# Kernel tuning notes

Measured on AMD Instinct MI355X. Metric: run time of the kernel, lower is better.

Reference implementation:

```python
import jax, jax.numpy as jnp
import numpy as np

H = 32        # num query heads
KVH = 8       # num kv heads
D = 128       # head_dim
ROPE_BASE = 10000.0
NEG_INF = jnp.finfo(jnp.float32).min


def rope_interleaved(x):
    """Interleaved (GPT-NeoX-style pairs (x0,x1),(x2,x3),...) RoPE. x: [b,s,h,d]."""
    d = x.shape[-1]
    inv_freq = 1.0 / (ROPE_BASE ** (jnp.arange(0, d, 2, dtype=jnp.float32) / d))  # [d/2]
    pos = jnp.arange(x.shape[1], dtype=jnp.float32)
    ang = pos[:, None] * inv_freq[None, :]                    # [s, d/2]
    cos = jnp.cos(ang)[None, :, None, :]
    sin = jnp.sin(ang)[None, :, None, :]
    xp = x.reshape(*x.shape[:-1], d // 2, 2)
    x1, x2 = xp[..., 0], xp[..., 1]
    r1 = x1 * cos - x2 * sin
    r2 = x1 * sin + x2 * cos
    return jnp.stack([r1, r2], axis=-1).reshape(x.shape)


def setup_inputs() -> dict:
    key = jax.random.key(0)
    k1, k2, k3 = jax.random.split(key, 3)
    B, S, E = 2, 2048, 4096
    x = jax.random.normal(k1, (B, S, E), dtype=jnp.float32)
    wqkv = jax.random.normal(k2, (E + 2 * KVH * D, E), dtype=jnp.float32) * 0.02
    wo = jax.random.normal(k3, (E, E), dtype=jnp.float32) * 0.02
    return {"x": x, "wqkv": wqkv, "wo": wo}


def reference(x, wqkv, wo):
    b, s, e = x.shape
    q_per_kv = H // KVH
    # fused QKV projection (torch Linear layout: y = x @ W.T)
    qkv = jnp.einsum('bse,fe->bsf', x, wqkv)
    # rearrange 'b s (h gs d) -> b s h gs d', gs = q_per_kv + 2
    qkv = qkv.reshape(b, s, KVH, q_per_kv + 2, D)
    q = qkv[..., :q_per_kv, :].reshape(b, s, H, D)   # (h gs) -> H query heads
    k = qkv[..., -2, :]                              # [b,s,KVH,D]
    v = qkv[..., -1, :]
    # RoPE (rotary_emb_dim == head_dim, interleaved)
    q = rope_interleaved(q)
    k = rope_interleaved(k)
    # GQA: expand kv heads to match query heads
    k = jnp.repeat(k, q_per_kv, axis=2)              # [b,s,H,D]
    v = jnp.repeat(v, q_per_kv, axis=2)
    scale = D ** -0.5
    scores = jnp.einsum('bqhd,bkhd->bhqk', q, k) * scale
    causal = jnp.tril(jnp.ones((s, s), dtype=bool))
    scores = jnp.where(causal[None, None], scores, NEG_INF)
    attn = jax.nn.softmax(scores, axis=-1)
    ctx = jnp.einsum('bhqk,bkhd->bqhd', attn, v).reshape(b, s, H * D)
    return jnp.einsum('bsf,ef->bse', ctx, wo)
```

## Files before the change

### kernel.cpp

```cpp
#include <hip/hip_runtime.h>
#include <cstdint>

typedef __bf16 bf16;
typedef __bf16 bf16x8 __attribute__((ext_vector_type(8)));
typedef float  f32x4  __attribute__((ext_vector_type(4)));

#define AS1(p) ((__attribute__((address_space(1))) void*)(p))
#define AS3(p) ((__attribute__((address_space(3))) void*)(p))

__device__ __forceinline__ void gload16(const void* g, void* l) {
  __builtin_amdgcn_global_load_lds(AS1(g), AS3(l), 16, 0, 0);
}

constexpr int B_ = 2, S_ = 2048, E_ = 4096, H_ = 32, KVH_ = 8, D_ = 128;
constexpr int QPK_ = H_ / KVH_;
constexpr int F_ = E_ + 2 * KVH_ * D_;
constexpr int M_ = B_ * S_;

__global__ void f2bf_k(const float* __restrict__ in, bf16* __restrict__ out, int n8) {
  int i = blockIdx.x * 256 + threadIdx.x;
  if (i >= n8) return;
  const float4* p = (const float4*)(in + (size_t)i * 8);
  float4 a = p[0], b = p[1];
  bf16x8 o;
  o[0] = (bf16)a.x; o[1] = (bf16)a.y; o[2] = (bf16)a.z; o[3] = (bf16)a.w;
  o[4] = (bf16)b.x; o[5] = (bf16)b.y; o[6] = (bf16)b.z; o[7] = (bf16)b.w;
  *(bf16x8*)(out + (size_t)i * 8) = o;
}

__global__ void rope_table_k(float2* __restrict__ tab) {
  int i = blockIdx.x * 256 + threadIdx.x;
  int s = i >> 6, f = i & 63;
  float inv = powf(10000.0f, -2.0f * (float)f / 128.0f);
  float ang = (float)s * inv;
  tab[i] = make_float2(cosf(ang), sinf(ang));
}

template <typename OutT>
__global__ __launch_bounds__(512, 2)
void gemm256(const bf16* __restrict__ A, const bf16* __restrict__ B,
             OutT* __restrict__ C, int M, int N, int K) {
  __shared__ bf16 As[2][16384];
  __shared__ bf16 Bs[2][16384];
  const int tid = threadIdx.x;
  const int wid = tid >> 6, lane = tid & 63;
  const int l15 = lane & 15, g = lane >> 4;
  const int wr = wid >> 2, wc = wid & 3;
  const int bm = blockIdx.x, bn = blockIdx.y;
  const bf16* Ab = A + (size_t)bm * 256 * K;
  const bf16* Bb = B + (size_t)bn * 256 * K;
  const int nT = K >> 6;
  const int swzr = (l15 & 7) << 4;

  f32x4 acc[8][4];
#pragma unroll
  for (int m = 0; m < 8; ++m)
#pragma unroll
    for (int n = 0; n < 4; ++n) acc[m][n] = (f32x4){0.f, 0.f, 0.f, 0.f};

  auto stg = [&](const bf16* src, bf16* dst, int t, int h) {
#pragma unroll
    for (int i = 0; i < 2; ++i) {
      int lb = h * 16384 + i * 8192 + wid * 1024 + lane * 16;
      int row = lb >> 7;
      int colb = (lb & 127) ^ ((row & 7) << 4);
      gload16(src + (size_t)row * K + t * 64 + (colb >> 1),
              dst + ((h * 16384 + i * 8192 + wid * 1024) >> 1));
    }
  };

  bf16x8 af[4][2];
  bf16x8 bfr[2][2][2];

  stg(Bb, Bs[0], 0, 0); stg(Bb, Bs[0], 0, 1);
  stg(Ab, As[0], 0, 0); stg(Ab, As[0], 0, 1);
  if (nT > 1) {
    stg(Bb, Bs[1], 1, 0); stg(Bb, Bs[1], 1, 1);
    asm volatile("s_waitcnt vmcnt(4)");
  } else {
    asm volatile("s_waitcnt vmcnt(0)");
  }
  __builtin_amdgcn_sched_barrier(0);
  __builtin_amdgcn_s_barrier();

  auto tileK = [&](int t, const int cur) {
#pragma unroll
    for (int m = 0; m < 4; ++m) {
      int arow = wr * 128 + m * 16 + l15;
#pragma unroll
      for (int ks = 0; ks < 2; ++ks)
        af[m][ks] = *(const bf16x8*)&As[cur][(arow << 6) + (((ks * 64 + g * 16) ^ swzr) >> 1)];
    }
#pragma unroll
    for (int n = 0; n < 2; ++n) {
      int brow = wc * 64 + n * 16 + l15;
#pragma unroll
      for (int ks = 0; ks < 2; ++ks)
        bfr[0][n][ks] = *(const bf16x8*)&Bs[cur][(brow << 6) + (((ks * 64 + g * 16) ^ swzr) >> 1)];
    }
    if (t + 1 < nT) stg(Ab, As[cur ^ 1], t + 1, 0);
    __builtin_amdgcn_s_barrier();
    asm volatile("s_waitcnt lgkmcnt(0)");
    __builtin_amdgcn_s_setprio(1);
#pragma unroll
    for (int ks = 0; ks < 2; ++ks)
#pragma unroll
      for (int m = 0; m < 4; ++m)
#pragma unroll
        for (int n = 0; n < 2; ++n)
          acc[m][n] = __builtin_amdgcn_mfma_f32_16x16x32_bf16(af[m][ks], bfr[0][n][ks], acc[m][n], 0, 0, 0);
    __builtin_amdgcn_s_setprio(0);
    __builtin_amdgcn_s_barrier();
#pragma unroll
    for (int n = 0; n < 2; ++n) {
      int brow = wc * 64 + 32 + n * 16 + l15;
#pragma unroll
      for (int ks = 0; ks < 2; ++ks)
        bfr[1][n][ks] = *(const bf16x8*)&Bs[cur][(brow << 6) + (((ks * 64 + g * 16) ^ swzr) >> 1)];
    }
    if (t + 1 < nT) stg(Ab, As[cur ^ 1], t + 1, 1);
    __builtin_amdgcn_s_barrier();
    asm volatile("s_waitcnt lgkmcnt(0)");
    __builtin_amdgcn_s_setprio(1);
#pragma unroll
    for (int ks = 0; ks < 2; ++ks)
#pragma unroll
      for (int m = 0; m < 4; ++m)
#pragma unroll
        for (int n = 0; n < 2; ++n)
          acc[m][2 + n] = __builtin_amdgcn_mfma_f32_16x16x32_bf16(af[m][ks], bfr[1][n][ks], acc[m][2 + n], 0, 0, 0);
    __builtin_amdgcn_s_setprio(0);
    __builtin_amdgcn_s_barrier();
#pragma unroll
    for (int m = 0; m < 4; ++m) {
      int arow = wr * 128 + 64 + m * 16 + l15;
#pragma unroll
      for (int ks = 0; ks < 2; ++ks)
        af[m][ks] = *(const bf16x8*)&As[cur][(arow << 6) + (((ks * 64 + g * 16) ^ swzr) >> 1)];
    }
    if (t + 2 < nT) stg(Bb, Bs[cur], t + 2, 0);
    __builtin_amdgcn_s_barrier();
    asm volatile("s_waitcnt lgkmcnt(0)");
    __builtin_amdgcn_s_setprio(1);
#pragma unroll
    for (int ks = 0; ks < 2; ++ks)
#pragma unroll
      for (int m = 0; m < 4; ++m)
#pragma unroll
        for (int n = 0; n < 2; ++n)
          acc[4 + m][n] = __builtin_amdgcn_mfma_f32_16x16x32_bf16(af[m][ks], bfr[0][n][ks], acc[4 + m][n], 0, 0, 0);
    __builtin_amdgcn_s_setprio(0);
    __builtin_amdgcn_s_barrier();
    if (t + 2 < nT) stg(Bb, Bs[cur], t + 2, 1);
    __builtin_amdgcn_s_setprio(1);
#pragma unroll
    for (int ks = 0; ks < 2; ++ks)
#pragma unroll
      for (int m = 0; m < 4; ++m)
#pragma unroll
        for (int n = 0; n < 2; ++n)
          acc[4 + m][2 + n] = __builtin_amdgcn_mfma_f32_16x16x32_bf16(af[m][ks], bfr[1][n][ks], acc[4 + m][2 + n], 0, 0, 0);
    __builtin_amdgcn_s_setprio(0);
    if (t + 2 < nT)      { asm volatile("s_waitcnt vmcnt(4)"); }
    else if (t + 1 < nT) { asm volatile("s_waitcnt vmcnt(0)"); }
    __builtin_amdgcn_sched_barrier(0);
    __builtin_amdgcn_s_barrier();
  };

  for (int tt = 0; tt < nT; tt += 2) {
    tileK(tt, 0);
    tileK(tt + 1, 1);
  }

#pragma unroll
  for (int mh = 0; mh < 2; ++mh)
#pragma unroll
    for (int m = 0; m < 4; ++m) {
      int row0 = bm * 256 + wr * 128 + mh * 64 + m * 16 + g * 4;
#pragma unroll
      for (int nh = 0; nh < 2; ++nh)
#pragma unroll
        for (int n = 0; n < 2; ++n) {
          int col = bn * 256 + wc * 64 + nh * 32 + n * 16 + l15;
          f32x4 v = acc[mh * 4 + m][nh * 2 + n];
#pragma unroll
          for (int r = 0; r < 4; ++r)
            C[(size_t)(row0 + r) * N + col] = (OutT)v[r];
        }
    }
}

__global__ void rope_q_k(const bf16* __restrict__ qkv, const float2* __restrict__ tab,
                         bf16* __restrict__ qout) {
  int idx = blockIdx.x * 256 + threadIdx.x;
  int c = idx & 15;
  int h = (idx >> 4) & 31;
  int s = (idx >> 9) & 2047;
  int b = idx >> 20;
  int d0 = c * 8;
  int kvh = h >> 2, j = h & 3;
  const bf16* src = qkv + (size_t)(b * 2048 + s) * F_ + kvh * (QPK_ + 2) * D_ + j * D_ + d0;
  bf16x8 v = *(const bf16x8*)src;
  const float2* tb = tab + s * 64 + (d0 >> 1);
  bf16x8 o;
#pragma unroll
  for (int p = 0; p < 4; ++p) {
    float x0 = (float)v[2 * p], x1 = (float)v[2 * p + 1];
    float2 cs = tb[p];
    o[2 * p]     = (bf16)(x0 * cs.x - x1 * cs.y);
    o[2 * p + 1] = (bf16)(x0 * cs.y + x1 * cs.x);
  }
  *(bf16x8*)(qout + (((size_t)b * 2048 + s) * 32 + h) * 128 + d0) = o;
}

__global__ void rope_k_k(const bf16* __restrict__ qkv, const float2* __restrict__ tab,
                         bf16* __restrict__ kout) {
  int idx = blockIdx.x * 256 + threadIdx.x;
  int c = idx & 15;
  int kvh = (idx >> 4) & 7;
  int s = (idx >> 7) & 2047;
  int b = idx >> 18;
  int d0 = c * 8;
  const bf16* src = qkv + (size_t)(b * 2048 + s) * F_ + kvh * (QPK_ + 2) * D_ + QPK_ * D_ + d0;
  bf16x8 v = *(const bf16x8*)src;
  const float2* tb = tab + s * 64 + (d0 >> 1);
  bf16x8 o;
#pragma unroll
  for (int p = 0; p < 4; ++p) {
    float x0 = (float)v[2 * p], x1 = (float)v[2 * p + 1];
    float2 cs = tb[p];
    o[2 * p]     = (bf16)(x0 * cs.x - x1 * cs.y);
    o[2 * p + 1] = (bf16)(x0 * cs.y + x1 * cs.x);
  }
  *(bf16x8*)(kout + ((size_t)(b * 8 + kvh) * 2048 + s) * 128 + d0) = o;
}

__global__ void vtrans_k(const bf16* __restrict__ qkv, bf16* __restrict__ vt) {
  int bidx = blockIdx.x;
  int st = bidx & 31;
  int dt = (bidx >> 5) & 3;
  int kvh = (bidx >> 7) & 7;
  int b = bidx >> 10;
  __shared__ bf16 tile[64][40];
  int t = threadIdx.x;
  {
    int sl = t >> 2, d0 = (t & 3) * 8;
    bf16x8 v = *(const bf16x8*)(qkv + (size_t)(b * 2048 + st * 64 + sl) * F_ +
                                kvh * (QPK_ + 2) * D_ + (QPK_ + 1) * D_ + dt * 32 + d0);
#pragma unroll
    for (int i = 0; i < 8; ++i) tile[sl][d0 + i] = v[i];
  }
  __syncthreads();
  {
    int dl = t >> 3, s0 = (t & 7) * 8;
    bf16x8 o;
#pragma unroll
    for (int i = 0; i < 8; ++i) o[i] = tile[s0 + i][dl];
    *(bf16x8*)(vt + ((size_t)(b * 8 + kvh) * 128 + dt * 32 + dl) * 2048 + st * 64 + s0) = o;
  }
}

__global__ __launch_bounds__(512, 2)
void attn_k(const bf16* __restrict__ q, const bf16* __restrict__ k,
            const bf16* __restrict__ vt, bf16* __restrict__ ctx) {
  int bid = blockIdx.x;
  bid = (bid & 7) * 64 + (bid >> 3);
  int qp = bid & 7;
  int h = (bid >> 3) & 31;
  int b = bid >> 8;
  int kvh = h >> 2;
  int tid = threadIdx.x, w = tid >> 6, lane = tid & 63;
  int l15 = lane & 15, g = lane >> 4;

  __shared__ bf16 Ks[3][64 * 128];
  __shared__ bf16 Vs[3][128 * 64];
  __shared__ bf16 Plds[8][16 * 80];

  bf16* Pw = &Plds[w][0];
  const float C2 = 0.08838834764831845f * 1.4426950408889634f;
  const float NEG = -3.0e38f;

  const bf16* kb_base = k + (size_t)(b * 8 + kvh) * 2048 * 128;
  const bf16* vt_base = vt + (size_t)(b * 8 + kvh) * 128 * 2048;

  auto stage = [&](int kv0, int buf) {
#pragma unroll
    for (int i = 0; i < 2; ++i) {
      int lt = i * 8192 + tid * 16;
      int row = lt >> 8;
      int ch = (lt >> 4) & 15;
      int srcel = (ch ^ (row & 7)) << 3;
      gload16(kb_base + (size_t)(kv0 + row) * 128 + srcel,
              &Ks[buf][(i * 8192 + w * 1024) >> 1]);
    }
#pragma unroll
    for (int i = 0; i < 2; ++i) {
      int lt = i * 8192 + tid * 16;
      int row = lt >> 7;
      int ch = (lt >> 4) & 7;
      int srcel = (ch ^ (row & 7)) << 3;
      gload16(vt_base + (size_t)row * 2048 + kv0 + srcel,
              &Vs[buf][(i * 8192 + w * 1024) >> 1]);
    }
  };

  const int kxor = (l15 & 7) << 4;

  for (int pass = 0; pass < 2; ++pass) {
    int qt = pass ? (15 - qp) : qp;
    int qrow0 = qt * 128 + w * 16;

    bf16x8 aq[4];
#pragma unroll
    for (int ks = 0; ks < 4; ++ks)
      aq[ks] = *(const bf16x8*)(q + (((size_t)b * 2048 + qrow0 + l15) * 32 + h) * 128 + ks * 32 + g * 8);

    f32x4 acco[8];
#pragma unroll
    for (int n = 0; n < 8; ++n) acco[n] = (f32x4){0.f, 0.f, 0.f, 0.f};
    float m_r[4] = {NEG, NEG, NEG, NEG};
    float l_r[4] = {0.f, 0.f, 0.f, 0.f};

    const int nk = 2 * qt + 2;
    stage(0, 0);
    stage(64, 1);
    asm volatile("s_waitcnt vmcnt(4)");
    __builtin_amdgcn_sched_barrier(0);
    __builtin_amdgcn_s_barrier();

    for (int kt = 0; kt < nk; ++kt) {
      int kv0 = kt * 64;
      int cur = kt % 3;
      if (kt + 2 < nk) stage(kv0 + 128, (kt + 2) % 3);

      if (kv0 <= qrow0 + 15) {
        f32x4 s[4];
#pragma unroll
        for (int n = 0; n < 4; ++n) s[n] = (f32x4){0.f, 0.f, 0.f, 0.f};
#pragma unroll
        for (int ks = 0; ks < 4; ++ks) {
          int off = ((ks * 64 + g * 16) ^ kxor) >> 1;
#pragma unroll
          for (int n = 0; n < 4; ++n) {
            bf16x8 kb = *(const bf16x8*)&Ks[cur][(n * 16 + l15) * 128 + off];
            s[n] = __builtin_amdgcn_mfma_f32_16x16x32_bf16(aq[ks], kb, s[n], 0, 0, 0);
          }
        }
        if (kv0 + 63 > qrow0) {
#pragma unroll
          for (int n = 0; n < 4; ++n)
#pragma unroll
            for (int r = 0; r < 4; ++r) {
              int qg = qrow0 + g * 4 + r;
              int kg = kv0 + n * 16 + l15;
              if (kg > qg) s[n][r] = NEG;
            }
        }
        float fac[4];
#pragma unroll
        for (int r = 0; r < 4; ++r) {
          float mx = fmaxf(fmaxf(s[0][r], s[1][r]), fmaxf(s[2][r], s[3][r]));
#pragma unroll
          for (int off = 1; off < 16; off <<= 1) mx = fmaxf(mx, __shfl_xor(mx, off));
          float mn = fmaxf(m_r[r], mx);
          fac[r] = exp2f((m_r[r] - mn) * C2);
          m_r[r] = mn;
        }
        float psum[4] = {0.f, 0.f, 0.f, 0.f};
#pragma unroll
        for (int n = 0; n < 4; ++n)
#pragma unroll
          for (int r = 0; r < 4; ++r) {
            float p = exp2f((s[n][r] - m_r[r]) * C2);
            psum[r] += p;
            Pw[(g * 4 + r) * 80 + n * 16 + l15] = (bf16)p;
          }
#pragma unroll
        for (int r = 0; r < 4; ++r) {
          float ps = psum[r];
#pragma unroll
          for (int off = 1; off < 16; off <<= 1) ps += __shfl_xor(ps, off);
          l_r[r] = l_r[r] * fac[r] + ps;
        }
#pragma unroll
        for (int n = 0; n < 8; ++n)
#pragma unroll
          for (int r = 0; r < 4; ++r) acco[n][r] *= fac[r];
        __builtin_amdgcn_sched_barrier(0);
        asm volatile("s_waitcnt lgkmcnt(0)");
        __builtin_amdgcn_sched_barrier(0);
#pragma unroll
        for (int ks = 0; ks < 2; ++ks) {
          bf16x8 pa = *(const bf16x8*)&Pw[l15 * 80 + ks * 32 + g * 8];
          int off = ((ks * 64 + g * 16) ^ kxor) >> 1;
#pragma unroll
          for (int n = 0; n < 8; ++n) {
            bf16x8 vb = *(const bf16x8*)&Vs[cur][(n * 16 + l15) * 64 + off];
            acco[n] = __builtin_amdgcn_mfma_f32_16x16x32_bf16(pa, vb, acco[n], 0, 0, 0);
          }
        }
      }

      if (kt + 1 < nk) {
        if (kt + 2 < nk) { asm volatile("s_waitcnt vmcnt(4)"); }
        else             { asm volatile("s_waitcnt vmcnt(0)"); }
        __builtin_amdgcn_sched_barrier(0);
      }
      __builtin_amdgcn_s_barrier();
    }

#pragma unroll
    for (int r = 0; r < 4; ++r) {
      float inv = 1.0f / l_r[r];
      int qg = qrow0 + g * 4 + r;
#pragma unroll
      for (int n = 0; n < 8; ++n)
        ctx[(((size_t)b * 2048 + qg) * 32 + h) * 128 + n * 16 + l15] = (bf16)(acco[n][r] * inv);
    }
  }
}

extern "C" void kernel_launch(void* const* d_in, const int* in_sizes, int n_in,
                              void* d_out, int out_size, void* d_ws, size_t ws_size,
                              hipStream_t stream) {
  const float* x = (const float*)d_in[0];
  const float* wqkv = (const float*)d_in[1];
  const float* wo = (const float*)d_in[2];
  float* out = (float*)d_out;
  char* ws = (char*)d_ws;

  bf16* xbf    = (bf16*)(ws + 0);
  bf16* wqkvbf = (bf16*)(ws + 33554432);
  bf16* qkvbf  = (bf16*)(ws + 83886080);
  bf16* qbuf   = (bf16*)(ws + 134217728);
  bf16* kbuf   = (bf16*)(ws + 167772160);
  bf16* vtbuf  = (bf16*)(ws + 176160768);
  float2* tab  = (float2*)(ws + 184549376);

  f2bf_k<<<8192, 256, 0, stream>>>(x, xbf, M_ * E_ / 8);
  f2bf_k<<<12288, 256, 0, stream>>>(wqkv, wqkvbf, F_ * E_ / 8);
  rope_table_k<<<512, 256, 0, stream>>>(tab);

  gemm256<bf16><<<dim3(M_ / 256, F_ / 256), 512, 0, stream>>>(xbf, wqkvbf, qkvbf, M_, F_, E_);

  rope_q_k<<<8192, 256, 0, stream>>>(qkvbf, tab, qbuf);
  rope_k_k<<<2048, 256, 0, stream>>>(qkvbf, tab, kbuf);
  vtrans_k<<<2048, 256, 0, stream>>>(qkvbf, vtbuf);

  bf16* wobf = qkvbf;
  f2bf_k<<<8192, 256, 0, stream>>>(wo, wobf, E_ * E_ / 8);

  bf16* ctx = xbf;
  attn_k<<<512, 512, 0, stream>>>(qbuf, kbuf, vtbuf, ctx);

  gemm256<float><<<dim3(M_ / 256, E_ / 256), 512, 0, stream>>>(ctx, wobf, out, M_, E_, E_);
}
```

Baseline: 590.0 us.

## Fuse init kernels, apply Q RoPE in GEMM epilogue, stream V from global

Merges the two fp32-to-bf16 conversions and the RoPE table build into one launch. Applies RoPE to Q heads directly in the QKV GEMM epilogue, using a lane shuffle to get the pair partner, which removes the separate rope_q pass over the QKV buffer. In attention, V is no longer staged through LDS; V fragments are read directly from global memory. K buffering drops to double-buffering and the launch bound is raised to 4 blocks, trading latency hiding for lower LDS use and higher occupancy. Waits become full vmcnt(0) drains each iteration, which may serialize loads.

Result: slower. 707.4 us (+19.9%).

```diff
diff --git a/kernel.cpp b/kernel.cpp
--- a/kernel.cpp
+++ b/kernel.cpp
@@ -17,9 +17,7 @@
 constexpr int F_ = E_ + 2 * KVH_ * D_;
 constexpr int M_ = B_ * S_;
 
-__global__ void f2bf_k(const float* __restrict__ in, bf16* __restrict__ out, int n8) {
-  int i = blockIdx.x * 256 + threadIdx.x;
-  if (i >= n8) return;
+__device__ __forceinline__ void conv8(const float* in, bf16* out, int i) {
   const float4* p = (const float4*)(in + (size_t)i * 8);
   float4 a = p[0], b = p[1];
   bf16x8 o;
@@ -28,18 +26,36 @@
   *(bf16x8*)(out + (size_t)i * 8) = o;
 }
 
-__global__ void rope_table_k(float2* __restrict__ tab) {
+__global__ void init_k(const float* __restrict__ x, bf16* __restrict__ xbf,
+                       const float* __restrict__ wqkv, bf16* __restrict__ wqkvbf,
+                       float2* __restrict__ tab) {
   int i = blockIdx.x * 256 + threadIdx.x;
-  int s = i >> 6, f = i & 63;
-  float inv = powf(10000.0f, -2.0f * (float)f / 128.0f);
-  float ang = (float)s * inv;
-  tab[i] = make_float2(cosf(ang), sinf(ang));
-}
-
-template <typename OutT>
+  if (i < 2097152) {
+    conv8(x, xbf, i);
+  } else if (i < 2097152 + 3145728) {
+    conv8(wqkv, wqkvbf, i - 2097152);
+  } else {
+    int j = i - 5242880;
+    if (j < 131072) {
+      int s = j >> 6, f = j & 63;
+      float inv = powf(10000.0f, -2.0f * (float)f / 128.0f);
+      float ang = (float)s * inv;
+      tab[j] = make_float2(cosf(ang), sinf(ang));
+    }
+  }
+}
+
+__global__ void f2bf_k(const float* __restrict__ in, bf16* __restrict__ out, int n8) {
+  int i = blockIdx.x * 256 + threadIdx.x;
+  if (i >= n8) return;
+  conv8(in, out, i);
+}
+
+template <bool FUSEQ, typename OutT>
 __global__ __launch_bounds__(512, 2)
 void gemm256(const bf16* __restrict__ A, const bf16* __restrict__ B,
-             OutT* __restrict__ C, int M, int N, int K) {
+             OutT* __restrict__ C, int M, int N, int K,
+             const float2* __restrict__ tab, bf16* __restrict__ qout) {
   __shared__ bf16 As[2][16384];
   __shared__ bf16 Bs[2][16384];
   const int tid = threadIdx.x;
@@ -172,45 +188,54 @@
     tileK(tt + 1, 1);
   }
 
-#pragma unroll
-  for (int mh = 0; mh < 2; ++mh)
-#pragma unroll
-    for (int m = 0; m < 4; ++m) {
-      int row0 = bm * 256 + wr * 128 + mh * 64 + m * 16 + g * 4;
-#pragma unroll
-      for (int nh = 0; nh < 2; ++nh)
-#pragma unroll
-        for (int n = 0; n < 2; ++n) {
-          int col = bn * 256 + wc * 64 + nh * 32 + n * 16 + l15;
-          f32x4 v = acc[mh * 4 + m][nh * 2 + n];
-#pragma unroll
-          for (int r = 0; r < 4; ++r)
-            C[(size_t)(row0 + r) * N + col] = (OutT)v[r];
-        }
-    }
-}
-
-__global__ void rope_q_k(const bf16* __restrict__ qkv, const float2* __restrict__ tab,
-                         bf16* __restrict__ qout) {
-  int idx = blockIdx.x * 256 + threadIdx.x;
-  int c = idx & 15;
-  int h = (idx >> 4) & 31;
-  int s = (idx >> 9) & 2047;
-  int b = idx >> 20;
-  int d0 = c * 8;
-  int kvh = h >> 2, j = h & 3;
-  const bf16* src = qkv + (size_t)(b * 2048 + s) * F_ + kvh * (QPK_ + 2) * D_ + j * D_ + d0;
-  bf16x8 v = *(const bf16x8*)src;
-  const float2* tb = tab + s * 64 + (d0 >> 1);
-  bf16x8 o;
-#pragma unroll
-  for (int p = 0; p < 4; ++p) {
-    float x0 = (float)v[2 * p], x1 = (float)v[2 * p + 1];
-    float2 cs = tb[p];
-    o[2 * p]     = (bf16)(x0 * cs.x - x1 * cs.y);
-    o[2 * p + 1] = (bf16)(x0 * cs.y + x1 * cs.x);
-  }
-  *(bf16x8*)(qout + (((size_t)b * 2048 + s) * 32 + h) * 128 + d0) = o;
+  if (FUSEQ && (bn % 3) < 2) {
+    const int r3 = bn % 3, kvh = bn / 3;
+#pragma unroll
+    for (int mh = 0; mh < 2; ++mh)
+#pragma unroll
+      for (int m = 0; m < 4; ++m) {
+        int srow = wr * 128 + mh * 64 + m * 16 + g * 4;
+#pragma unroll
+        for (int nh = 0; nh < 2; ++nh)
+#pragma unroll
+          for (int n = 0; n < 2; ++n) {
+            int colt = wc * 64 + nh * 32 + n * 16 + l15;
+            int hj = r3 * 2 + (colt >> 7);
+            int d = colt & 127;
+            int f = d >> 1;
+            f32x4 v = acc[mh * 4 + m][nh * 2 + n];
+            f32x4 vp;
+#pragma unroll
+            for (int r = 0; r < 4; ++r) vp[r] = __shfl_xor(v[r], 1);
+#pragma unroll
+            for (int r = 0; r < 4; ++r) {
+              int grow = bm * 256 + srow + r;
+              int pos = grow & 2047, bb = grow >> 11;
+              float2 cs = tab[pos * 64 + f];
+              float o = (l15 & 1) ? (vp[r] * cs.y + v[r] * cs.x)
+                                  : (v[r] * cs.x - vp[r] * cs.y);
+              qout[(((size_t)bb * 2048 + pos) * 32 + kvh * 4 + hj) * 128 + d] = (bf16)o;
+            }
+          }
+      }
+  } else {
+#pragma unroll
+    for (int mh = 0; mh < 2; ++mh)
+#pragma unroll
+      for (int m = 0; m < 4; ++m) {
+        int row0 = bm * 256 + wr * 128 + mh * 64 + m * 16 + g * 4;
+#pragma unroll
+        for (int nh = 0; nh < 2; ++nh)
+#pragma unroll
+          for (int n = 0; n < 2; ++n) {
+            int col = bn * 256 + wc * 64 + nh * 32 + n * 16 + l15;
+            f32x4 v = acc[mh * 4 + m][nh * 2 + n];
+#pragma unroll
+            for (int r = 0; r < 4; ++r)
+              C[(size_t)(row0 + r) * N + col] = (OutT)v[r];
+          }
+      }
+  }
 }
 
 __global__ void rope_k_k(const bf16* __restrict__ qkv, const float2* __restrict__ tab,
@@ -260,7 +285,7 @@
   }
 }
 
-__global__ __launch_bounds__(512, 2)
+__global__ __launch_bounds__(512, 4)
 void attn_k(const bf16* __restrict__ q, const bf16* __restrict__ k,
             const bf16* __restrict__ vt, bf16* __restrict__ ctx) {
   int bid = blockIdx.x;
@@ -272,8 +297,7 @@
   int tid = threadIdx.x, w = tid >> 6, lane = tid & 63;
   int l15 = lane & 15, g = lane >> 4;
 
-  __shared__ bf16 Ks[3][64 * 128];
-  __shared__ bf16 Vs[3][128 * 64];
+  __shared__ bf16 Ks[2][64 * 128];
   __shared__ bf16 Plds[8][16 * 80];
 
   bf16* Pw = &Plds[w][0];
@@ -283,7 +307,7 @@
   const bf16* kb_base = k + (size_t)(b * 8 + kvh) * 2048 * 128;
   const bf16* vt_base = vt + (size_t)(b * 8 + kvh) * 128 * 2048;
 
-  auto stage = [&](int kv0, int buf) {
+  auto stageK = [&](int kv0, int buf) {
 #pragma unroll
     for (int i = 0; i < 2; ++i) {
       int lt = i * 8192 + tid * 16;
@@ -293,15 +317,6 @@
       gload16(kb_base + (size_t)(kv0 + row) * 128 + srcel,
               &Ks[buf][(i * 8192 + w * 1024) >> 1]);
     }
-#pragma unroll
-    for (int i = 0; i < 2; ++i) {
-      int lt = i * 8192 + tid * 16;
-      int row = lt >> 7;
-      int ch = (lt >> 4) & 7;
-      int srcel = (ch ^ (row & 7)) << 3;
-      gload16(vt_base + (size_t)row * 2048 + kv0 + srcel,
-              &Vs[buf][(i * 8192 + w * 1024) >> 1]);
-    }
   };
 
   const int kxor = (l15 & 7) << 4;
@@ -322,16 +337,15 @@
     float l_r[4] = {0.f, 0.f, 0.f, 0.f};
 
     const int nk = 2 * qt + 2;
-    stage(0, 0);
-    stage(64, 1);
-    asm volatile("s_waitcnt vmcnt(4)");
+    stageK(0, 0);
+    asm volatile("s_waitcnt vmcnt(0)");
     __builtin_amdgcn_sched_barrier(0);
     __builtin_amdgcn_s_barrier();
 
     for (int kt = 0; kt < nk; ++kt) {
       int kv0 = kt * 64;
-      int cur = kt % 3;
-      if (kt + 2 < nk) stage(kv0 + 128, (kt + 2) % 3);
+      int cur = kt & 1;
+      if (kt + 1 < nk) stageK(kv0 + 64, cur ^ 1);
 
       if (kv0 <= qrow0 + 15) {
         f32x4 s[4];
@@ -392,20 +406,17 @@
 #pragma unroll
         for (int ks = 0; ks < 2; ++ks) {
           bf16x8 pa = *(const bf16x8*)&Pw[l15 * 80 + ks * 32 + g * 8];
-          int off = ((ks * 64 + g * 16) ^ kxor) >> 1;
 #pragma unroll
           for (int n = 0; n < 8; ++n) {
-            bf16x8 vb = *(const bf16x8*)&Vs[cur][(n * 16 + l15) * 64 + off];
+            bf16x8 vb = *(const bf16x8*)(vt_base + (size_t)(n * 16 + l15) * 2048 + kv0 + ks * 32 + g * 8);
             acco[n] = __builtin_amdgcn_mfma_f32_16x16x32_bf16(pa, vb, acco[n], 0, 0, 0);
           }
         }
       }
 
-      if (kt + 1 < nk) {
-        if (kt + 2 < nk) { asm volatile("s_waitcnt vmcnt(4)"); }
-        else             { asm volatile("s_waitcnt vmcnt(0)"); }
-        __builtin_amdgcn_sched_barrier(0);
-      }
+      asm volatile("s_waitcnt lgkmcnt(0)");
+      asm volatile("s_waitcnt vmcnt(0)");
+      __builtin_amdgcn_sched_barrier(0);
       __builtin_amdgcn_s_barrier();
     }
 
@@ -417,6 +428,7 @@
       for (int n = 0; n < 8; ++n)
         ctx[(((size_t)b * 2048 + qg) * 32 + h) * 128 + n * 16 + l15] = (bf16)(acco[n][r] * inv);
     }
+    __builtin_amdgcn_s_barrier();
   }
 }
 
@@ -437,13 +449,11 @@
   bf16* vtbuf  = (bf16*)(ws + 176160768);
   float2* tab  = (float2*)(ws + 184549376);
 
-  f2bf_k<<<8192, 256, 0, stream>>>(x, xbf, M_ * E_ / 8);
-  f2bf_k<<<12288, 256, 0, stream>>>(wqkv, wqkvbf, F_ * E_ / 8);
-  rope_table_k<<<512, 256, 0, stream>>>(tab);
-
-  gemm256<bf16><<<dim3(M_ / 256, F_ / 256), 512, 0, stream>>>(xbf, wqkvbf, qkvbf, M_, F_, E_);
-
-  rope_q_k<<<8192, 256, 0, stream>>>(qkvbf, tab, qbuf);
+  init_k<<<20992, 256, 0, stream>>>(x, xbf, wqkv, wqkvbf, tab);
+
+  gemm256<true, bf16><<<dim3(M_ / 256, F_ / 256), 512, 0, stream>>>(
+      xbf, wqkvbf, qkvbf, M_, F_, E_, tab, qbuf);
+
   rope_k_k<<<2048, 256, 0, stream>>>(qkvbf, tab, kbuf);
   vtrans_k<<<2048, 256, 0, stream>>>(qkvbf, vtbuf);
 
@@ -453,5 +463,6 @@
   bf16* ctx = xbf;
   attn_k<<<512, 512, 0, stream>>>(qbuf, kbuf, vtbuf, ctx);
 
-  gemm256<float><<<dim3(M_ / 256, E_ / 256), 512, 0, stream>>>(ctx, wobf, out, M_, E_, E_);
-}
+  gemm256<false, float><<<dim3(M_ / 256, E_ / 256), 512, 0, stream>>>(
+      ctx, wobf, out, M_, E_, E_, tab, nullptr);
+}
```
